# Optimization experiments

Hardware: AMD Instinct MI355X
Metric: run time of the kernel (lower is better)

## Reference

```python
import jax, jax.numpy as jnp
import numpy as np

VOXEL_SIZE = jnp.array([0.075, 0.075], dtype=jnp.float32)
PC_RANGE = jnp.array([-54.0, -54.0], dtype=jnp.float32)
FUSION_STRIDE = 8.0
SRC_STRIDES = (4.0, 8.0)
RADII = (2.4, 4.8)
NSAMPLE = 16
NKEY = 500


def _mlp(x, w1, g1, b1, w2, b2):
    # Linear(no bias) + BatchNorm(eval, running mean=0/var=1 -> affine) + ReLU, then Linear
    h = jax.nn.relu((x @ w1) * g1 + b1)
    return h @ w2 + b2


def _world(coords, stride):
    # voxel coord -> world xy center
    return (coords.astype(jnp.float32) + 0.5) * stride * VOXEL_SIZE + PC_RANGE


def _gather_rows(x, idx):
    # x: (B, N, ...), idx: (B, ...) -> per-batch row gather
    return jax.vmap(lambda f, i: f[i])(x, idx)


def _knn(key_world, src_world, src_feat, radius):
    # key_world (B,Nk,2), src_world (B,Ns,2), src_feat (B,Ns,C)
    d2 = jnp.sum((key_world[:, :, None, :] - src_world[:, None, :, :]) ** 2, axis=-1)  # (B,Nk,Ns)
    d2 = jnp.where(d2 <= radius * radius, d2, jnp.inf)
    negd, idx = jax.lax.top_k(-d2, NSAMPLE)  # nearest NSAMPLE within radius, (B,Nk,K)
    valid = jnp.isfinite(negd).astype(src_feat.dtype)  # empty==0 mask
    feats = _gather_rows(src_feat, idx)  # (B,Nk,K,C)
    return feats * valid[..., None]


def setup_inputs() -> dict:
    key = jax.random.key(0)
    ks = jax.random.split(key, 24)
    s = 0.05
    return {
        'fusion_feat': jax.random.normal(ks[0], (2, 20000, 128), jnp.float32),
        'src_feat_a': jax.random.normal(ks[1], (2, 30000, 128), jnp.float32),
        'src_feat_b': jax.random.normal(ks[2], (2, 30000, 128), jnp.float32),
        'heat_w1': jax.random.normal(ks[3], (128, 128), jnp.float32) * s,
        'heat_g1': jnp.ones((128,), jnp.float32),
        'heat_b1': jnp.zeros((128,), jnp.float32),
        'heat_w2': jax.random.normal(ks[4], (128, 10), jnp.float32) * s,
        'heat_b2': jnp.zeros((10,), jnp.float32),
        'knn_w': jax.random.normal(ks[5], (2, 16), jnp.float32) * s,
        'knn_b': jnp.zeros((2,), jnp.float32),
        'kw_w1': jax.random.normal(ks[6], (128, 64), jnp.float32) * s,
        'kw_g1': jnp.ones((64,), jnp.float32),
        'kw_b1': jnp.zeros((64,), jnp.float32),
        'kw_w2': jax.random.normal(ks[7], (64, 3), jnp.float32) * s,
        'kw_b2': jnp.zeros((3,), jnp.float32),
        'fuse_w1': jax.random.normal(ks[8], (256, 256), jnp.float32) * s,
        'fuse_g1': jnp.ones((256,), jnp.float32),
        'fuse_b1': jnp.zeros((256,), jnp.float32),
        'fuse_w2': jax.random.normal(ks[9], (256, 128), jnp.float32) * s,
        'fuse_b2': jnp.zeros((128,), jnp.float32),
        'fusion_coords': jax.random.randint(ks[10], (2, 20000, 2), 0, 180, jnp.int32),
        'src_coords_a': jax.random.randint(ks[11], (2, 30000, 2), 0, 360, jnp.int32),
        'src_coords_b': jax.random.randint(ks[12], (2, 30000, 2), 0, 180, jnp.int32),
    }


def reference(fusion_feat, src_feat_a, src_feat_b, heat_w1, heat_g1, heat_b1,
              heat_w2, heat_b2, knn_w, knn_b, kw_w1, kw_g1, kw_b1, kw_w2, kw_b2,
              fuse_w1, fuse_g1, fuse_b1, fuse_w2, fuse_b2,
              fusion_coords, src_coords_a, src_coords_b):
    B = fusion_feat.shape[0]
    # heatmap head over all fusion voxels
    scores10 = _mlp(fusion_feat, heat_w1, heat_g1, heat_b1, heat_w2, heat_b2)  # (B,Nf,10)
    heat_scores = jnp.max(scores10, axis=-1)
    cls = jnp.argmax(scores10, axis=-1)
    # per-sample top-k key voxel selection
    _, tki = jax.lax.top_k(jax.nn.sigmoid(heat_scores), NKEY)  # (B,Nk)
    key_feat = _gather_rows(fusion_feat, tki)      # (B,Nk,128)
    key_coords = _gather_rows(fusion_coords, tki)  # (B,Nk,2)
    key_class = _gather_rows(cls, tki)             # (B,Nk)
    key_world = _world(key_coords, FUSION_STRIDE)  # (B,Nk,2)

    srcs = ((src_feat_a, src_coords_a), (src_feat_b, src_coords_b))
    mlp_feats = []
    for s, (sf, sc) in enumerate(srcs):
        sw = _world(sc, SRC_STRIDES[s])
        kf = _knn(key_world, sw, sf, RADII[s])  # (B,Nk,K,C), zeroed where empty
        # Linear over the K neighbor axis (knn_feat_mlp: NSAMPLE -> 1)
        mf = jnp.einsum('bnkc,k->bnc', kf, knn_w[s]) + knn_b[s]
        mlp_feats.append(mf)

    w = jax.nn.softmax(_mlp(key_feat, kw_w1, kw_g1, kw_b1, kw_w2, kw_b2), axis=-1)  # (B,Nk,3)
    # faithful to original: key_voxel_feat is re-scaled cumulatively inside the loop
    kvf = key_feat
    fuse_sum = jnp.zeros_like(key_feat)
    for i in range(len(srcs)):
        kvf = w[..., i:i + 1] * kvf
        fuse_sum = fuse_sum + kvf * mlp_feats[i]
    fused = jnp.concatenate([fuse_sum, kvf], axis=-1)  # (B,Nk,256)
    out = _mlp(fused, fuse_w1, fuse_g1, fuse_b1, fuse_w2, fuse_b2)  # (B,Nk,128)

    bs_col = jnp.broadcast_to(jnp.arange(B, dtype=key_coords.dtype)[:, None, None], (B, NKEY, 1))
    key_voxel_indices = jnp.concatenate([bs_col, key_coords], axis=-1).reshape(B * NKEY, 3)
    return (out.reshape(B * NKEY, -1), key_voxel_indices,
            heat_scores.reshape(-1), scores10.reshape(-1, scores10.shape[-1]), key_class)
```

## Files before the change

### kernel.cpp

```cpp
#include <hip/hip_runtime.h>
#include <math.h>

#define BB 2
#define NF 20000
#define NS 30000
#define CH 128
#define NK 500
#define KNN 16
#define KPB 4

#define HA 2.4024f
#define HB 4.8048f
#define NCA 45
#define NCB 23
#define CELLS_A 2025
#define CELLS_B 529

#define OUT0_OFF 0
#define OUT1_OFF 128000
#define OUT2_OFF 131000
#define OUT3_OFF 171000
#define OUT4_OFF 571000

#define WS_CLS   0
#define WS_TKI   160000
#define WS_KW    164000
#define WS_MF    172000
#define WS_KEYS  WS_MF
#define WS_GSTART 1196000
#define WS_PTS    1236880
#define WS_PIDX   2196880

#define STB(s,b)  ((s) ? (4052 + (b) * 530) : ((b) * 2026))

__device__ __forceinline__ void fma4(float4& acc, float sc, const float4& wv) {
    acc.x += sc * wv.x; acc.y += sc * wv.y;
    acc.z += sc * wv.z; acc.w += sc * wv.w;
}

__device__ __forceinline__ unsigned ordf(float s) {
    unsigned u = __float_as_uint(s);
    return (u & 0x80000000u) ? ~u : (u | 0x80000000u);
}

__global__ __launch_bounds__(256) void heat_kernel(
    const float* __restrict__ x,
    const float* __restrict__ w1,
    const float* __restrict__ g1, const float* __restrict__ b1,
    const float* __restrict__ w2,
    const float* __restrict__ b2,
    float* __restrict__ out_heat,
    float* __restrict__ out_s10,
    int* __restrict__ cls,
    unsigned long long* __restrict__ keys)
{
    __shared__ float As[64 * 72];
    __shared__ float Ws[64 * 132];
    __shared__ float W2s[1280];
    const int tid = threadIdx.x;
    const int m0 = blockIdx.x * 64;
    const int tx = tid & 15;
    const int ty = tid >> 4;

    for (int v = tid; v < 1280; v += 256) W2s[v] = w2[v];

    float acc[4][8];
#pragma unroll
    for (int i = 0; i < 4; ++i)
#pragma unroll
        for (int j = 0; j < 8; ++j) acc[i][j] = 0.f;

    const float4* xv = (const float4*)x;
    const float4* w1v = (const float4*)w1;

    for (int kc = 0; kc < 128; kc += 64) {
#pragma unroll
        for (int i = 0; i < 4; ++i) {
            int v = tid + i * 256;
            int row = v >> 4, c4 = v & 15;
            float4 val = xv[(size_t)(m0 + row) * 32 + (kc >> 2) + c4];
            *(float4*)&As[row * 72 + c4 * 4] = val;
        }
#pragma unroll
        for (int i = 0; i < 8; ++i) {
            int v = tid + i * 256;
            int k = v >> 5, c4 = v & 31;
            float4 val = w1v[(size_t)(kc + k) * 32 + c4];
            *(float4*)&Ws[k * 132 + c4 * 4] = val;
        }
        __syncthreads();

        const float* a0p = &As[(ty * 4 + 0) * 72];
        const float* a1p = &As[(ty * 4 + 1) * 72];
        const float* a2p = &As[(ty * 4 + 2) * 72];
        const float* a3p = &As[(ty * 4 + 3) * 72];
#pragma unroll 4
        for (int k = 0; k < 64; ++k) {
            float4 bA = *(const float4*)&Ws[k * 132 + tx * 8];
            float4 bB = *(const float4*)&Ws[k * 132 + tx * 8 + 4];
            float a0 = a0p[k], a1 = a1p[k], a2 = a2p[k], a3 = a3p[k];
            acc[0][0] += a0 * bA.x; acc[0][1] += a0 * bA.y; acc[0][2] += a0 * bA.z; acc[0][3] += a0 * bA.w;
            acc[0][4] += a0 * bB.x; acc[0][5] += a0 * bB.y; acc[0][6] += a0 * bB.z; acc[0][7] += a0 * bB.w;
            acc[1][0] += a1 * bA.x; acc[1][1] += a1 * bA.y; acc[1][2] += a1 * bA.z; acc[1][3] += a1 * bA.w;
            acc[1][4] += a1 * bB.x; acc[1][5] += a1 * bB.y; acc[1][6] += a1 * bB.z; acc[1][7] += a1 * bB.w;
            acc[2][0] += a2 * bA.x; acc[2][1] += a2 * bA.y; acc[2][2] += a2 * bA.z; acc[2][3] += a2 * bA.w;
            acc[2][4] += a2 * bB.x; acc[2][5] += a2 * bB.y; acc[2][6] += a2 * bB.z; acc[2][7] += a2 * bB.w;
            acc[3][0] += a3 * bA.x; acc[3][1] += a3 * bA.y; acc[3][2] += a3 * bA.z; acc[3][3] += a3 * bA.w;
            acc[3][4] += a3 * bB.x; acc[3][5] += a3 * bB.y; acc[3][6] += a3 * bB.z; acc[3][7] += a3 * bB.w;
        }
        __syncthreads();
    }

    float4 g1a = ((const float4*)g1)[tx * 2], g1b = ((const float4*)g1)[tx * 2 + 1];
    float4 b1a = ((const float4*)b1)[tx * 2], b1b = ((const float4*)b1)[tx * 2 + 1];
    float* Hs = Ws;
#pragma unroll
    for (int i = 0; i < 4; ++i) {
        int row = ty * 4 + i;
        float4 hA, hB;
        hA.x = fmaxf(acc[i][0] * g1a.x + b1a.x, 0.f);
        hA.y = fmaxf(acc[i][1] * g1a.y + b1a.y, 0.f);
        hA.z = fmaxf(acc[i][2] * g1a.z + b1a.z, 0.f);
        hA.w = fmaxf(acc[i][3] * g1a.w + b1a.w, 0.f);
        hB.x = fmaxf(acc[i][4] * g1b.x + b1b.x, 0.f);
        hB.y = fmaxf(acc[i][5] * g1b.y + b1b.y, 0.f);
        hB.z = fmaxf(acc[i][6] * g1b.z + b1b.z, 0.f);
        hB.w = fmaxf(acc[i][7] * g1b.w + b1b.w, 0.f);
        *(float4*)&Hs[row * 132 + tx * 8] = hA;
        *(float4*)&Hs[row * 132 + tx * 8 + 4] = hB;
    }
    __syncthreads();

    const int r = tid >> 2;
    const int p = tid & 3;
    float a2[10];
#pragma unroll
    for (int c = 0; c < 10; ++c) a2[c] = 0.f;
    for (int kk = 0; kk < 32; ++kk) {
        int k = kk * 4 + p;
        float hv = Hs[r * 132 + k];
#pragma unroll
        for (int c = 0; c < 10; ++c) a2[c] += hv * W2s[k * 10 + c];
    }
#pragma unroll
    for (int c = 0; c < 10; ++c) {
        a2[c] += __shfl_xor(a2[c], 1);
        a2[c] += __shfl_xor(a2[c], 2);
    }
    if (p == 0) {
        int m = m0 + r;
        float best = -INFINITY;
        int bi = 0;
#pragma unroll
        for (int c = 0; c < 10; ++c) {
            float s = a2[c] + b2[c];
            out_s10[(size_t)m * 10 + c] = s;
            if (s > best) { best = s; bi = c; }
        }
        out_heat[m] = best;
        cls[m] = bi;
        int b = m / NF;
        unsigned i = (unsigned)(m - b * NF);
        float sig = 1.0f / (1.0f + expf(-best));
        keys[m] = ((unsigned long long)ordf(sig) << 32) | (unsigned)(~i);
    }
}

#define H1BINS 16384
#define H2BINS 1024

__device__ __forceinline__ void world_cell_sb(
    const int2* sc, int s, int i, float& sx, float& sy, int& cell)
{
    int2 c = sc[i];
    float stride = s ? 8.0f : 4.0f;
    sx = __fadd_rn(__fmul_rn(__fmul_rn(__fadd_rn((float)c.x, 0.5f), stride), 0.075f), -54.0f);
    sy = __fadd_rn(__fmul_rn(__fmul_rn(__fadd_rn((float)c.y, 0.5f), stride), 0.075f), -54.0f);
    float inv_h = s ? (1.0f / HB) : (1.0f / HA);
    int nc = s ? NCB : NCA;
    int cx = (int)floorf((sx + 54.0f) * inv_h);
    int cy = (int)floorf((sy + 54.0f) * inv_h);
    cx = min(max(cx, 0), nc - 1);
    cy = min(max(cy, 0), nc - 1);
    cell = cy * nc + cx;
}

__global__ __launch_bounds__(1024) void mid_kernel(
    const unsigned long long* __restrict__ keys,
    const int* __restrict__ cls,
    const int* __restrict__ fcoords,
    float* __restrict__ out1,
    float* __restrict__ out4,
    int* __restrict__ tki,
    float* __restrict__ keyworld,
    const int* __restrict__ sca, const int* __restrict__ scb,
    int* __restrict__ gstart,
    float2* __restrict__ pts, int* __restrict__ pidx)
{
    __shared__ unsigned h[H1BINS];
    __shared__ unsigned long long list[1024];
    __shared__ unsigned csum[1024];
    __shared__ unsigned ssum[32];
    __shared__ unsigned sel_s, krem_s, cnt_s;
    __shared__ int ghist[2048];
    __shared__ int gt0[1024], gt1[1024];
    const int tid = threadIdx.x;
    const int blk = blockIdx.x;

    if (blk >= 2) {
        const int s = (blk - 2) >> 1, b = (blk - 2) & 1;
        const int n = s ? CELLS_B : CELLS_A;
        const int stb = STB(s, b);
        const int2* sc = ((const int2*)(s ? scb : sca)) + (size_t)b * NS;
        const size_t pbase = ((size_t)s * BB + b) * NS;

        for (int i = tid; i < 2048; i += 1024) ghist[i] = 0;
        __syncthreads();
        for (int i = tid; i < NS; i += 1024) {
            float sx, sy; int cell;
            world_cell_sb(sc, s, i, sx, sy, cell);
            atomicAdd(&ghist[cell], 1);
        }
        __syncthreads();
        int i0 = tid * 2, i1 = tid * 2 + 1;
        int c0 = (i0 < n) ? ghist[i0] : 0;
        int c1 = (i1 < n) ? ghist[i1] : 0;
        gt0[tid] = c0 + c1;
        __syncthreads();
        int* srcp = gt0; int* dstp = gt1;
        for (int off = 1; off < 1024; off <<= 1) {
            int v = srcp[tid];
            if (tid >= off) v += srcp[tid - off];
            dstp[tid] = v;
            __syncthreads();
            int* tmp = srcp; srcp = dstp; dstp = tmp;
        }
        int excl = (tid == 0) ? 0 : srcp[tid - 1];
        if (i0 < n) { gstart[stb + i0] = excl; ghist[i0] = excl; }
        if (i1 < n) { gstart[stb + i1] = excl + c0; ghist[i1] = excl + c0; }
        if (tid == 0) gstart[stb + n] = NS;
        __syncthreads();
        for (int i = tid; i < NS; i += 1024) {
            float sx, sy; int cell;
            world_cell_sb(sc, s, i, sx, sy, cell);
            int pos = atomicAdd(&ghist[cell], 1);
            pts[pbase + pos] = make_float2(sx, sy);
            pidx[pbase + pos] = i;
        }
        return;
    }

    const int b = blk;
    const unsigned long long* kb = keys + (size_t)b * NF;

    for (int i = tid; i < H1BINS; i += 1024) h[i] = 0u;
    __syncthreads();
#pragma unroll 4
    for (int i = tid; i < NF; i += 1024)
        atomicAdd(&h[(unsigned)(kb[i] >> 50)], 1u);
    __syncthreads();
    {
        unsigned s = 0;
        int base = tid * 16;
#pragma unroll
        for (int j = 0; j < 16; ++j) s += h[base + j];
        csum[tid] = s;
    }
    __syncthreads();
    if (tid < 32) {
        unsigned s = 0;
        for (int j = 0; j < 32; ++j) s += csum[tid * 32 + j];
        ssum[tid] = s;
    }
    __syncthreads();
    if (tid == 0) {
        unsigned K = NK, acc = 0;
        int sidx = 31;
        for (; sidx > 0; --sidx) { if (acc + ssum[sidx] >= K) break; acc += ssum[sidx]; }
        int cidx = sidx * 32 + 31;
        for (;; --cidx) { if (acc + csum[cidx] >= K) break; acc += csum[cidx]; }
        int bin = cidx * 16 + 15;
        for (;; --bin) { if (acc + h[bin] >= K) break; acc += h[bin]; }
        sel_s = (unsigned)bin;
        krem_s = K - acc;
    }
    __syncthreads();
    const unsigned T1 = sel_s;
    const unsigned K2 = krem_s;

    for (int i = tid; i < H2BINS; i += 1024) h[i] = 0u;
    __syncthreads();
#pragma unroll 4
    for (int i = tid; i < NF; i += 1024) {
        unsigned long long key = kb[i];
        if ((unsigned)(key >> 50) == T1)
            atomicAdd(&h[(unsigned)(key >> 40) & 1023u], 1u);
    }
    __syncthreads();
    if (tid < 32) {
        unsigned s = 0;
        for (int j = 0; j < 32; ++j) s += h[tid * 32 + j];
        csum[tid] = s;
    }
    __syncthreads();
    if (tid == 0) {
        unsigned acc = 0;
        int cidx = 31;
        for (; cidx > 0; --cidx) { if (acc + csum[cidx] >= K2) break; acc += csum[cidx]; }
        int bin = cidx * 32 + 31;
        for (;; --bin) { if (acc + h[bin] >= K2) break; acc += h[bin]; }
        sel_s = (T1 << 10) | (unsigned)bin;
        cnt_s = 0u;
    }
    __syncthreads();
    const unsigned thr24 = sel_s;

#pragma unroll 4
    for (int i = tid; i < NF; i += 1024) {
        unsigned long long key = kb[i];
        if ((unsigned)(key >> 40) >= thr24) {
            unsigned pos = atomicAdd(&cnt_s, 1u);
            if (pos < 1024u) list[pos] = key;
        }
    }
    __syncthreads();
    unsigned cc = cnt_s > 1024u ? 1024u : cnt_s;
    if ((unsigned)tid >= cc) list[tid] = 0ull;
    __syncthreads();

    for (int kk = 2; kk <= 1024; kk <<= 1) {
        for (int j = kk >> 1; j > 0; j >>= 1) {
            int i = tid, ixj = i ^ j;
            if (ixj > i) {
                unsigned long long a = list[i], bv = list[ixj];
                bool up = ((i & kk) == 0);
                if (up ? (a < bv) : (a > bv)) { list[i] = bv; list[ixj] = a; }
            }
            __syncthreads();
        }
    }

    if (tid < NK) {
        unsigned long long key = list[tid];
        int idx = (int)(~(unsigned)(key & 0xFFFFFFFFull));
        tki[b * NK + tid] = idx;
        int c0 = fcoords[((size_t)b * NF + idx) * 2 + 0];
        int c1 = fcoords[((size_t)b * NF + idx) * 2 + 1];
        size_t o = (size_t)(b * NK + tid);
        out1[o * 3 + 0] = (float)b;
        out1[o * 3 + 1] = (float)c0;
        out1[o * 3 + 2] = (float)c1;
        float wx = __fadd_rn(__fmul_rn(__fmul_rn(__fadd_rn((float)c0, 0.5f), 8.0f), 0.075f), -54.0f);
        float wy = __fadd_rn(__fmul_rn(__fmul_rn(__fadd_rn((float)c1, 0.5f), 8.0f), 0.075f), -54.0f);
        keyworld[o * 2 + 0] = wx;
        keyworld[o * 2 + 1] = wy;
        out4[o] = (float)cls[(size_t)b * NF + idx];
    }
}

__global__ __launch_bounds__(256) void knn_kernel(
    const float* __restrict__ sfa, const float* __restrict__ sfb,
    const int* __restrict__ gstart,
    const float2* __restrict__ pts, const int* __restrict__ pidx,
    const float* __restrict__ knn_w,
    const float* __restrict__ knn_b,
    const float* __restrict__ keyworld,
    float* __restrict__ mf)
{
    __shared__ unsigned long long list[1024];
    __shared__ float psum[128];
    __shared__ unsigned cnt_s;
    const int tid = threadIdx.x;
    const int blk = blockIdx.x;
    const int s = blk / (BB * NK);
    const int rest = blk % (BB * NK);
    const int b = rest / NK;
    const int r = rest % NK;
    const float* sfeat = s ? sfb : sfa;
    const float r2 = s ? (float)(4.8 * 4.8) : (float)(2.4 * 2.4);
    const float inv_h = s ? (1.0f / HB) : (1.0f / HA);
    const int nc = s ? NCB : NCA;
    const int stb = STB(s, b);
    const size_t pbase = ((size_t)s * BB + b) * NS;

    if (tid == 0) cnt_s = 0u;
    __syncthreads();
    const float kx = keyworld[((size_t)b * NK + r) * 2 + 0];
    const float ky = keyworld[((size_t)b * NK + r) * 2 + 1];
    int cx = (int)floorf((kx + 54.0f) * inv_h);
    int cy = (int)floorf((ky + 54.0f) * inv_h);
    cx = min(max(cx, 0), nc - 1);
    cy = min(max(cy, 0), nc - 1);
    const int c0 = max(cx - 1, 0), c1 = min(cx + 1, nc - 1);
    const int cy0 = max(cy - 1, 0), cy1 = min(cy + 1, nc - 1);

    for (int cyy = cy0; cyy <= cy1; ++cyy) {
        int lo = gstart[stb + cyy * nc + c0];
        int hi = gstart[stb + cyy * nc + c1 + 1];
        for (int p = lo + tid; p < hi; p += 256) {
            float2 w = pts[pbase + p];
            float dx = __fsub_rn(kx, w.x);
            float dy = __fsub_rn(ky, w.y);
            float d2 = __fadd_rn(__fmul_rn(dx, dx), __fmul_rn(dy, dy));
            if (d2 <= r2) {
                unsigned pos = atomicAdd(&cnt_s, 1u);
                if (pos < 1024u)
                    list[pos] = ((unsigned long long)__float_as_uint(d2) << 32)
                              | (unsigned)pidx[pbase + p];
            }
        }
    }
    __syncthreads();
    int cc = (int)cnt_s;
    if (cc > 1024) cc = 1024;
    int n2 = 16;
    while (n2 < cc) n2 <<= 1;
    for (int i = tid; i < n2; i += 256)
        if (i >= cc) list[i] = ~0ull;
    __syncthreads();
    for (int kk = 2; kk <= n2; kk <<= 1) {
        for (int j = kk >> 1; j > 0; j >>= 1) {
            for (int i = tid; i < n2; i += 256) {
                int ixj = i ^ j;
                if (ixj > i) {
                    unsigned long long a = list[i], bv = list[ixj];
                    bool up = ((i & kk) == 0);
                    bool sw = up ? (a > bv) : (a < bv);
                    if (sw) { list[i] = bv; list[ixj] = a; }
                }
            }
            __syncthreads();
        }
    }
    {
        int K = cc < KNN ? cc : KNN;
        int col = tid & 127, half = tid >> 7;
        float acc = 0.f;
        int k0 = half * 8, k1 = min(K, half * 8 + 8);
        for (int k = k0; k < k1; ++k) {
            unsigned i = (unsigned)(list[k] & 0xFFFFFFFFull);
            acc += knn_w[s * 16 + k] * sfeat[((size_t)b * NS + i) * CH + col];
        }
        if (half) psum[col] = acc;
        __syncthreads();
        if (!half)
            mf[(((size_t)s * BB + b) * NK + r) * CH + col] = knn_b[s] + acc + psum[col];
    }
}

__global__ __launch_bounds__(1024) void fuse_kernel(
    const float* __restrict__ ffeat,
    const int* __restrict__ tki,
    const float* __restrict__ kw_w1, const float* __restrict__ kw_g1,
    const float* __restrict__ kw_b1, const float* __restrict__ kw_w2,
    const float* __restrict__ kw_b2,
    const float* __restrict__ fuse_w1, const float* __restrict__ fuse_g1,
    const float* __restrict__ fuse_b1, const float* __restrict__ fuse_w2,
    const float* __restrict__ fuse_b2,
    const float* __restrict__ mf,
    float* __restrict__ out0)
{
    __shared__ float pL[16384];
    __shared__ float xsT[512];
    __shared__ float mfs[1024];
    __shared__ float fusedvT[1024];
    __shared__ float h2sT[1024];
    __shared__ float prm[964];
    __shared__ float hsX[256];
    __shared__ float p2[96];
    __shared__ float l3[12];
    __shared__ float wsm[8];
    __shared__ int idxs[KPB], bs[KPB], rs[KPB];
    const int tid = threadIdx.x;
    const int f0 = blockIdx.x * KPB;

    if (tid < 964) {
        float v;
        if (tid < 64)       v = kw_g1[tid];
        else if (tid < 128) v = kw_b1[tid - 64];
        else if (tid < 320) v = kw_w2[tid - 128];
        else if (tid < 323) v = kw_b2[tid - 320];
        else if (tid < 324) v = 0.f;
        else if (tid < 580) v = fuse_g1[tid - 324];
        else if (tid < 836) v = fuse_b1[tid - 580];
        else                v = fuse_b2[tid - 836];
        prm[tid] = v;
    }
    if (tid < KPB) {
        int flat = f0 + tid;
        int b = flat / NK;
        bs[tid] = b;
        rs[tid] = flat - b * NK;
        idxs[tid] = tki[flat];
    }
    __syncthreads();

    if (tid < 128) {
        int key = tid >> 5, c4 = tid & 31;
        float4 v = ((const float4*)(ffeat + ((size_t)bs[key] * NF + idxs[key]) * CH))[c4];
        xsT[(c4 * 4 + 0) * 4 + key] = v.x;
        xsT[(c4 * 4 + 1) * 4 + key] = v.y;
        xsT[(c4 * 4 + 2) * 4 + key] = v.z;
        xsT[(c4 * 4 + 3) * 4 + key] = v.w;
    }
    if (tid < 256) {
        int ss = tid >> 7, key = (tid >> 5) & 3, c4 = tid & 31;
        float4 v = ((const float4*)(mf + (((size_t)ss * BB + bs[key]) * NK + rs[key]) * CH))[c4];
        *(float4*)&mfs[ss * 512 + key * 128 + c4 * 4] = v;
    }
    __syncthreads();

    if (tid < 256) {
        const int og = tid & 15, kseg = tid >> 4;
        float4 wr[8];
#pragma unroll
        for (int m = 0; m < 8; ++m)
            wr[m] = ((const float4*)kw_w1)[(kseg * 8 + m) * 16 + og];
        float4 a0 = {0, 0, 0, 0}, a1 = {0, 0, 0, 0}, a2 = {0, 0, 0, 0}, a3 = {0, 0, 0, 0};
#pragma unroll
        for (int m = 0; m < 8; ++m) {
            float4 f4 = *(const float4*)&xsT[(kseg * 8 + m) * 4];
            fma4(a0, f4.x, wr[m]);
            fma4(a1, f4.y, wr[m]);
            fma4(a2, f4.z, wr[m]);
            fma4(a3, f4.w, wr[m]);
        }
        *(float4*)&pL[(kseg * 4 + 0) * 64 + og * 4] = a0;
        *(float4*)&pL[(kseg * 4 + 1) * 64 + og * 4] = a1;
        *(float4*)&pL[(kseg * 4 + 2) * 64 + og * 4] = a2;
        *(float4*)&pL[(kseg * 4 + 3) * 64 + og * 4] = a3;
    }
    __syncthreads();
    if (tid < 256) {
        int out = tid >> 2, key = tid & 3;
        float s = 0.f;
#pragma unroll
        for (int ks = 0; ks < 16; ++ks) s += pL[(ks * 4 + key) * 64 + out];
        float t = s * prm[out] + prm[64 + out];
        hsX[key * 64 + out] = t > 0.f ? t : 0.f;
    }
    __syncthreads();
    if (tid < 96) {
        int key = tid / 24, rr = tid % 24, out = rr >> 3, seg = rr & 7;
        float acc = 0.f;
#pragma unroll
        for (int m = 0; m < 8; ++m) {
            int k = seg * 8 + m;
            acc += hsX[key * 64 + k] * prm[128 + k * 3 + out];
        }
        p2[(key * 3 + out) * 8 + seg] = acc;
    }
    __syncthreads();
    if (tid < 12) {
        int key = tid / 3, out = tid % 3;
        float s = 0.f;
#pragma unroll
        for (int j = 0; j < 8; ++j) s += p2[(key * 3 + out) * 8 + j];
        l3[key * 3 + out] = s + prm[320 + out];
    }
    __syncthreads();
    if (tid < KPB) {
        float l0 = l3[tid * 3], l1 = l3[tid * 3 + 1], l2 = l3[tid * 3 + 2];
        float m = fmaxf(l0, fmaxf(l1, l2));
        float e0 = expf(l0 - m), e1 = expf(l1 - m), e2 = expf(l2 - m);
        float sum = e0 + e1 + e2;
        wsm[tid * 2 + 0] = e0 / sum;
        wsm[tid * 2 + 1] = e1 / sum;
    }
    __syncthreads();

    {
        int c = tid >> 2, key = tid & 3;
        float w0 = wsm[key * 2], w1_ = wsm[key * 2 + 1];
        float val;
        if (c < 128) {
            float xv_ = xsT[c * 4 + key];
            float m0 = mfs[key * 128 + c];
            float m1 = mfs[512 + key * 128 + c];
            float kv = w0 * xv_;
            float kv2 = w1_ * kv;
            val = kv * m0 + kv2 * m1;
        } else {
            float xv_ = xsT[(c - 128) * 4 + key];
            val = w1_ * (w0 * xv_);
        }
        fusedvT[tid] = val;
    }
    __syncthreads();

    {
        const int og = tid & 63, kseg = tid >> 6;
        const float4* w1v = (const float4*)fuse_w1;
        float4 wr[16];
#pragma unroll
        for (int m = 0; m < 16; ++m)
            wr[m] = w1v[(kseg * 16 + m) * 64 + og];
        float4 a0 = {0, 0, 0, 0}, a1 = {0, 0, 0, 0}, a2 = {0, 0, 0, 0}, a3 = {0, 0, 0, 0};
#pragma unroll
        for (int m = 0; m < 16; ++m) {
            float4 f4 = *(const float4*)&fusedvT[(kseg * 16 + m) * 4];
            fma4(a0, f4.x, wr[m]);
            fma4(a1, f4.y, wr[m]);
            fma4(a2, f4.z, wr[m]);
            fma4(a3, f4.w, wr[m]);
        }
        *(float4*)&pL[(kseg * 4 + 0) * 256 + og * 4] = a0;
        *(float4*)&pL[(kseg * 4 + 1) * 256 + og * 4] = a1;
        *(float4*)&pL[(kseg * 4 + 2) * 256 + og * 4] = a2;
        *(float4*)&pL[(kseg * 4 + 3) * 256 + og * 4] = a3;
    }
    __syncthreads();
    {
        int out = tid >> 2, key = tid & 3;
        float s = 0.f;
#pragma unroll
        for (int ks = 0; ks < 16; ++ks) s += pL[(ks * 4 + key) * 256 + out];
        float t = s * prm[324 + out] + prm[580 + out];
        h2sT[out * 4 + key] = t > 0.f ? t : 0.f;
    }
    __syncthreads();

    {
        const int og2 = tid & 31, kseg2 = tid >> 5;
        const float4* w2v = (const float4*)fuse_w2;
        float4 wr[8];
#pragma unroll
        for (int m = 0; m < 8; ++m)
            wr[m] = w2v[(kseg2 * 8 + m) * 32 + og2];
        float4 a0 = {0, 0, 0, 0}, a1 = {0, 0, 0, 0}, a2 = {0, 0, 0, 0}, a3 = {0, 0, 0, 0};
#pragma unroll
        for (int m = 0; m < 8; ++m) {
            float4 f4 = *(const float4*)&h2sT[(kseg2 * 8 + m) * 4];
            fma4(a0, f4.x, wr[m]);
            fma4(a1, f4.y, wr[m]);
            fma4(a2, f4.z, wr[m]);
            fma4(a3, f4.w, wr[m]);
        }
        *(float4*)&pL[(kseg2 * 4 + 0) * 128 + og2 * 4] = a0;
        *(float4*)&pL[(kseg2 * 4 + 1) * 128 + og2 * 4] = a1;
        *(float4*)&pL[(kseg2 * 4 + 2) * 128 + og2 * 4] = a2;
        *(float4*)&pL[(kseg2 * 4 + 3) * 128 + og2 * 4] = a3;
    }
    __syncthreads();
    if (tid < 512) {
        int out = tid >> 2, key = tid & 3;
        float s = prm[836 + out];
#pragma unroll
        for (int ks = 0; ks < 32; ++ks) s += pL[(ks * 4 + key) * 128 + out];
        out0[((size_t)bs[key] * NK + rs[key]) * CH + out] = s;
    }
}

extern "C" void kernel_launch(void* const* d_in, const int* in_sizes, int n_in,
                              void* d_out, int out_size, void* d_ws, size_t ws_size,
                              hipStream_t stream)
{
    const float* fusion_feat = (const float*)d_in[0];
    const float* src_feat_a  = (const float*)d_in[1];
    const float* src_feat_b  = (const float*)d_in[2];
    const float* heat_w1 = (const float*)d_in[3];
    const float* heat_g1 = (const float*)d_in[4];
    const float* heat_b1 = (const float*)d_in[5];
    const float* heat_w2 = (const float*)d_in[6];
    const float* heat_b2 = (const float*)d_in[7];
    const float* knn_w   = (const float*)d_in[8];
    const float* knn_b   = (const float*)d_in[9];
    const float* kw_w1   = (const float*)d_in[10];
    const float* kw_g1   = (const float*)d_in[11];
    const float* kw_b1   = (const float*)d_in[12];
    const float* kw_w2   = (const float*)d_in[13];
    const float* kw_b2   = (const float*)d_in[14];
    const float* fuse_w1 = (const float*)d_in[15];
    const float* fuse_g1 = (const float*)d_in[16];
    const float* fuse_b1 = (const float*)d_in[17];
    const float* fuse_w2 = (const float*)d_in[18];
    const float* fuse_b2 = (const float*)d_in[19];
    const int* fusion_coords = (const int*)d_in[20];
    const int* src_coords_a  = (const int*)d_in[21];
    const int* src_coords_b  = (const int*)d_in[22];

    float* out = (float*)d_out;
    char* ws = (char*)d_ws;
    int* cls = (int*)(ws + WS_CLS);
    int* tki = (int*)(ws + WS_TKI);
    float* keyworld = (float*)(ws + WS_KW);
    float* mf = (float*)(ws + WS_MF);
    unsigned long long* keys = (unsigned long long*)(ws + WS_KEYS);
    int* gstart = (int*)(ws + WS_GSTART);
    float2* pts = (float2*)(ws + WS_PTS);
    int* pidx = (int*)(ws + WS_PIDX);

    heat_kernel<<<(BB * NF) / 64, 256, 0, stream>>>(
        fusion_feat, heat_w1, heat_g1, heat_b1, heat_w2, heat_b2,
        out + OUT2_OFF, out + OUT3_OFF, cls, keys);

    mid_kernel<<<6, 1024, 0, stream>>>(
        keys, cls, fusion_coords,
        out + OUT1_OFF, out + OUT4_OFF, tki, keyworld,
        src_coords_a, src_coords_b, gstart, pts, pidx);

    knn_kernel<<<2 * BB * NK, 256, 0, stream>>>(
        src_feat_a, src_feat_b, gstart, pts, pidx,
        knn_w, knn_b, keyworld, mf);

    fuse_kernel<<<(BB * NK) / KPB, 1024, 0, stream>>>(
        fusion_feat, tki, kw_w1, kw_g1, kw_b1, kw_w2, kw_b2,
        fuse_w1, fuse_g1, fuse_b1, fuse_w2, fuse_b2, mf, out + OUT0_OFF);
}
```

Baseline: 245.3 us.

## Move grid-binning into heat kernel and streamline top-k selection

The source-point grid binning (histogram, scan, scatter) moves out of the serial mid kernel into four extra blocks of the heat kernel, so it overlaps with the heat MLP instead of running after it. The top-k kernel now finds the threshold bin with a parallel suffix scan instead of serial loops. It skips the second histogram pass when the first-level candidates fit in the list. It also replaces the 1024-element bitonic sort with a rank-by-count placement over the candidates. This shortens the latency-bound single-block section between kernels, but the binning now runs with 256 threads per block instead of 1024. The O(n^2) ranking assumes distinct keys.

```diff
diff --git a/kernel.cpp b/kernel.cpp
--- a/kernel.cpp
+++ b/kernel.cpp
@@ -33,6 +33,8 @@
 
 #define STB(s,b)  ((s) ? (4052 + (b) * 530) : ((b) * 2026))
 
+#define HEATBLKS 625
+
 __device__ __forceinline__ void fma4(float4& acc, float sc, const float4& wv) {
     acc.x += sc * wv.x; acc.y += sc * wv.y;
     acc.z += sc * wv.z; acc.w += sc * wv.w;
@@ -41,6 +43,22 @@
 __device__ __forceinline__ unsigned ordf(float s) {
     unsigned u = __float_as_uint(s);
     return (u & 0x80000000u) ? ~u : (u | 0x80000000u);
+}
+
+__device__ __forceinline__ void world_cell_sb(
+    const int2* sc, int s, int i, float& sx, float& sy, int& cell)
+{
+    int2 c = sc[i];
+    float stride = s ? 8.0f : 4.0f;
+    sx = __fadd_rn(__fmul_rn(__fmul_rn(__fadd_rn((float)c.x, 0.5f), stride), 0.075f), -54.0f);
+    sy = __fadd_rn(__fmul_rn(__fmul_rn(__fadd_rn((float)c.y, 0.5f), stride), 0.075f), -54.0f);
+    float inv_h = s ? (1.0f / HB) : (1.0f / HA);
+    int nc = s ? NCB : NCA;
+    int cx = (int)floorf((sx + 54.0f) * inv_h);
+    int cy = (int)floorf((sy + 54.0f) * inv_h);
+    cx = min(max(cx, 0), nc - 1);
+    cy = min(max(cy, 0), nc - 1);
+    cell = cy * nc + cx;
 }
 
 __global__ __launch_bounds__(256) void heat_kernel(
@@ -52,12 +70,69 @@
     float* __restrict__ out_heat,
     float* __restrict__ out_s10,
     int* __restrict__ cls,
-    unsigned long long* __restrict__ keys)
+    unsigned long long* __restrict__ keys,
+    const int* __restrict__ sca, const int* __restrict__ scb,
+    int* __restrict__ gstart,
+    float2* __restrict__ pts, int* __restrict__ pidx)
 {
     __shared__ float As[64 * 72];
     __shared__ float Ws[64 * 132];
     __shared__ float W2s[1280];
     const int tid = threadIdx.x;
+
+    if (blockIdx.x >= HEATBLKS) {
+        const int g = blockIdx.x - HEATBLKS;
+        const int s = g >> 1, b = g & 1;
+        const int n = s ? CELLS_B : CELLS_A;
+        const int stb = STB(s, b);
+        const int2* sc = ((const int2*)(s ? scb : sca)) + (size_t)b * NS;
+        const size_t pbase = ((size_t)s * BB + b) * NS;
+        int* ghist = (int*)As;
+        int* ct  = (int*)Ws;
+        int* ct2 = ((int*)Ws) + 256;
+
+        for (int i = tid; i < 2048; i += 256) ghist[i] = 0;
+        __syncthreads();
+        for (int i = tid; i < NS; i += 256) {
+            float sx, sy; int cell;
+            world_cell_sb(sc, s, i, sx, sy, cell);
+            atomicAdd(&ghist[cell], 1);
+        }
+        __syncthreads();
+        const int base = tid * 8;
+        int loc[8]; int csum8 = 0;
+#pragma unroll
+        for (int j = 0; j < 8; ++j) { loc[j] = ghist[base + j]; csum8 += loc[j]; }
+        ct[tid] = csum8;
+        __syncthreads();
+        int* srcp = ct; int* dstp = ct2;
+        for (int off = 1; off < 256; off <<= 1) {
+            int v = srcp[tid];
+            if (tid >= off) v += srcp[tid - off];
+            dstp[tid] = v;
+            __syncthreads();
+            int* t = srcp; srcp = dstp; dstp = t;
+        }
+        int excl = (tid == 0) ? 0 : srcp[tid - 1];
+        __syncthreads();
+#pragma unroll
+        for (int j = 0; j < 8; ++j) {
+            if (base + j < n) gstart[stb + base + j] = excl;
+            ghist[base + j] = excl;
+            excl += loc[j];
+        }
+        if (tid == 0) gstart[stb + n] = NS;
+        __syncthreads();
+        for (int i = tid; i < NS; i += 256) {
+            float sx, sy; int cell;
+            world_cell_sb(sc, s, i, sx, sy, cell);
+            int pos = atomicAdd(&ghist[cell], 1);
+            pts[pbase + pos] = make_float2(sx, sy);
+            pidx[pbase + pos] = i;
+        }
+        return;
+    }
+
     const int m0 = blockIdx.x * 64;
     const int tx = tid & 15;
     const int ty = tid >> 4;
@@ -167,91 +242,24 @@
 }
 
 #define H1BINS 16384
-#define H2BINS 1024
-
-__device__ __forceinline__ void world_cell_sb(
-    const int2* sc, int s, int i, float& sx, float& sy, int& cell)
-{
-    int2 c = sc[i];
-    float stride = s ? 8.0f : 4.0f;
-    sx = __fadd_rn(__fmul_rn(__fmul_rn(__fadd_rn((float)c.x, 0.5f), stride), 0.075f), -54.0f);
-    sy = __fadd_rn(__fmul_rn(__fmul_rn(__fadd_rn((float)c.y, 0.5f), stride), 0.075f), -54.0f);
-    float inv_h = s ? (1.0f / HB) : (1.0f / HA);
-    int nc = s ? NCB : NCA;
-    int cx = (int)floorf((sx + 54.0f) * inv_h);
-    int cy = (int)floorf((sy + 54.0f) * inv_h);
-    cx = min(max(cx, 0), nc - 1);
-    cy = min(max(cy, 0), nc - 1);
-    cell = cy * nc + cx;
-}
-
-__global__ __launch_bounds__(1024) void mid_kernel(
+
+__global__ __launch_bounds__(1024) void topk_kernel(
     const unsigned long long* __restrict__ keys,
     const int* __restrict__ cls,
     const int* __restrict__ fcoords,
     float* __restrict__ out1,
     float* __restrict__ out4,
     int* __restrict__ tki,
-    float* __restrict__ keyworld,
-    const int* __restrict__ sca, const int* __restrict__ scb,
-    int* __restrict__ gstart,
-    float2* __restrict__ pts, int* __restrict__ pidx)
+    float* __restrict__ keyworld)
 {
     __shared__ unsigned h[H1BINS];
+    __shared__ unsigned sA[1024], sB[1024];
     __shared__ unsigned long long list[1024];
-    __shared__ unsigned csum[1024];
-    __shared__ unsigned ssum[32];
-    __shared__ unsigned sel_s, krem_s, cnt_s;
-    __shared__ int ghist[2048];
-    __shared__ int gt0[1024], gt1[1024];
+    __shared__ unsigned chunk_s, aboveC_s, T1_s, aboveT1_s, cand_s, thr_s, cnt_s;
+    const int b = blockIdx.x;
     const int tid = threadIdx.x;
-    const int blk = blockIdx.x;
-
-    if (blk >= 2) {
-        const int s = (blk - 2) >> 1, b = (blk - 2) & 1;
-        const int n = s ? CELLS_B : CELLS_A;
-        const int stb = STB(s, b);
-        const int2* sc = ((const int2*)(s ? scb : sca)) + (size_t)b * NS;
-        const size_t pbase = ((size_t)s * BB + b) * NS;
-
-        for (int i = tid; i < 2048; i += 1024) ghist[i] = 0;
-        __syncthreads();
-        for (int i = tid; i < NS; i += 1024) {
-            float sx, sy; int cell;
-            world_cell_sb(sc, s, i, sx, sy, cell);
-            atomicAdd(&ghist[cell], 1);
-        }
-        __syncthreads();
-        int i0 = tid * 2, i1 = tid * 2 + 1;
-        int c0 = (i0 < n) ? ghist[i0] : 0;
-        int c1 = (i1 < n) ? ghist[i1] : 0;
-        gt0[tid] = c0 + c1;
-        __syncthreads();
-        int* srcp = gt0; int* dstp = gt1;
-        for (int off = 1; off < 1024; off <<= 1) {
-            int v = srcp[tid];
-            if (tid >= off) v += srcp[tid - off];
-            dstp[tid] = v;
-            __syncthreads();
-            int* tmp = srcp; srcp = dstp; dstp = tmp;
-        }
-        int excl = (tid == 0) ? 0 : srcp[tid - 1];
-        if (i0 < n) { gstart[stb + i0] = excl; ghist[i0] = excl; }
-        if (i1 < n) { gstart[stb + i1] = excl + c0; ghist[i1] = excl + c0; }
-        if (tid == 0) gstart[stb + n] = NS;
-        __syncthreads();
-        for (int i = tid; i < NS; i += 1024) {
-            float sx, sy; int cell;
-            world_cell_sb(sc, s, i, sx, sy, cell);
-            int pos = atomicAdd(&ghist[cell], 1);
-            pts[pbase + pos] = make_float2(sx, sy);
-            pidx[pbase + pos] = i;
-        }
-        return;
-    }
-
-    const int b = blk;
     const unsigned long long* kb = keys + (size_t)b * NF;
+    const unsigned K = NK;
 
     for (int i = tid; i < H1BINS; i += 1024) h[i] = 0u;
     __syncthreads();
@@ -259,102 +267,110 @@
     for (int i = tid; i < NF; i += 1024)
         atomicAdd(&h[(unsigned)(kb[i] >> 50)], 1u);
     __syncthreads();
+    unsigned ck = 0;
     {
-        unsigned s = 0;
         int base = tid * 16;
 #pragma unroll
-        for (int j = 0; j < 16; ++j) s += h[base + j];
-        csum[tid] = s;
-    }
-    __syncthreads();
-    if (tid < 32) {
-        unsigned s = 0;
-        for (int j = 0; j < 32; ++j) s += csum[tid * 32 + j];
-        ssum[tid] = s;
+        for (int j = 0; j < 16; ++j) ck += h[base + j];
+        sA[tid] = ck;
+    }
+    __syncthreads();
+    unsigned* srcp = sA; unsigned* dstp = sB;
+    for (int off = 1; off < 1024; off <<= 1) {
+        unsigned v = srcp[tid];
+        if (tid + off < 1024) v += srcp[tid + off];
+        dstp[tid] = v;
+        __syncthreads();
+        unsigned* t = srcp; srcp = dstp; dstp = t;
+    }
+    {
+        unsigned suf = srcp[tid];
+        unsigned above = suf - ck;
+        if (above < K && K <= suf) { chunk_s = (unsigned)tid; aboveC_s = above; }
     }
     __syncthreads();
     if (tid == 0) {
-        unsigned K = NK, acc = 0;
-        int sidx = 31;
-        for (; sidx > 0; --sidx) { if (acc + ssum[sidx] >= K) break; acc += ssum[sidx]; }
-        int cidx = sidx * 32 + 31;
-        for (;; --cidx) { if (acc + csum[cidx] >= K) break; acc += csum[cidx]; }
-        int bin = cidx * 16 + 15;
+        int bin = (int)chunk_s * 16 + 15;
+        unsigned acc = aboveC_s;
         for (;; --bin) { if (acc + h[bin] >= K) break; acc += h[bin]; }
-        sel_s = (unsigned)bin;
-        krem_s = K - acc;
-    }
-    __syncthreads();
-    const unsigned T1 = sel_s;
-    const unsigned K2 = krem_s;
-
-    for (int i = tid; i < H2BINS; i += 1024) h[i] = 0u;
-    __syncthreads();
+        T1_s = (unsigned)bin;
+        aboveT1_s = acc;
+        cand_s = acc + h[bin];
+        cnt_s = 0u;
+    }
+    __syncthreads();
+    const unsigned T1 = T1_s;
+
+    if (cand_s <= 1024u) {
 #pragma unroll 4
-    for (int i = tid; i < NF; i += 1024) {
-        unsigned long long key = kb[i];
-        if ((unsigned)(key >> 50) == T1)
-            atomicAdd(&h[(unsigned)(key >> 40) & 1023u], 1u);
-    }
-    __syncthreads();
-    if (tid < 32) {
-        unsigned s = 0;
-        for (int j = 0; j < 32; ++j) s += h[tid * 32 + j];
-        csum[tid] = s;
-    }
-    __syncthreads();
-    if (tid == 0) {
-        unsigned acc = 0;
-        int cidx = 31;
-        for (; cidx > 0; --cidx) { if (acc + csum[cidx] >= K2) break; acc += csum[cidx]; }
-        int bin = cidx * 32 + 31;
-        for (;; --bin) { if (acc + h[bin] >= K2) break; acc += h[bin]; }
-        sel_s = (T1 << 10) | (unsigned)bin;
-        cnt_s = 0u;
-    }
-    __syncthreads();
-    const unsigned thr24 = sel_s;
-
+        for (int i = tid; i < NF; i += 1024) {
+            unsigned long long key = kb[i];
+            if ((unsigned)(key >> 50) >= T1) {
+                unsigned pos = atomicAdd(&cnt_s, 1u);
+                if (pos < 1024u) list[pos] = key;
+            }
+        }
+    } else {
+        const unsigned K2 = K - aboveT1_s;
+        h[tid] = 0u;
+        __syncthreads();
 #pragma unroll 4
-    for (int i = tid; i < NF; i += 1024) {
-        unsigned long long key = kb[i];
-        if ((unsigned)(key >> 40) >= thr24) {
-            unsigned pos = atomicAdd(&cnt_s, 1u);
-            if (pos < 1024u) list[pos] = key;
-        }
-    }
-    __syncthreads();
-    unsigned cc = cnt_s > 1024u ? 1024u : cnt_s;
-    if ((unsigned)tid >= cc) list[tid] = 0ull;
-    __syncthreads();
-
-    for (int kk = 2; kk <= 1024; kk <<= 1) {
-        for (int j = kk >> 1; j > 0; j >>= 1) {
-            int i = tid, ixj = i ^ j;
-            if (ixj > i) {
-                unsigned long long a = list[i], bv = list[ixj];
-                bool up = ((i & kk) == 0);
-                if (up ? (a < bv) : (a > bv)) { list[i] = bv; list[ixj] = a; }
+        for (int i = tid; i < NF; i += 1024) {
+            unsigned long long key = kb[i];
+            if ((unsigned)(key >> 50) == T1)
+                atomicAdd(&h[(unsigned)(key >> 40) & 1023u], 1u);
+        }
+        __syncthreads();
+        unsigned hb = h[tid];
+        sA[tid] = hb;
+        __syncthreads();
+        unsigned* s2 = sA; unsigned* d2 = sB;
+        for (int off = 1; off < 1024; off <<= 1) {
+            unsigned v = s2[tid];
+            if (tid + off < 1024) v += s2[tid + off];
+            d2[tid] = v;
+            __syncthreads();
+            unsigned* t = s2; s2 = d2; d2 = t;
+        }
+        {
+            unsigned suf = s2[tid];
+            unsigned above = suf - hb;
+            if (above < K2 && K2 <= suf) thr_s = (T1 << 10) | (unsigned)tid;
+        }
+        __syncthreads();
+        const unsigned thr24 = thr_s;
+#pragma unroll 4
+        for (int i = tid; i < NF; i += 1024) {
+            unsigned long long key = kb[i];
+            if ((unsigned)(key >> 40) >= thr24) {
+                unsigned pos = atomicAdd(&cnt_s, 1u);
+                if (pos < 1024u) list[pos] = key;
             }
-            __syncthreads();
-        }
-    }
-
-    if (tid < NK) {
-        unsigned long long key = list[tid];
-        int idx = (int)(~(unsigned)(key & 0xFFFFFFFFull));
-        tki[b * NK + tid] = idx;
-        int c0 = fcoords[((size_t)b * NF + idx) * 2 + 0];
-        int c1 = fcoords[((size_t)b * NF + idx) * 2 + 1];
-        size_t o = (size_t)(b * NK + tid);
-        out1[o * 3 + 0] = (float)b;
-        out1[o * 3 + 1] = (float)c0;
-        out1[o * 3 + 2] = (float)c1;
-        float wx = __fadd_rn(__fmul_rn(__fmul_rn(__fadd_rn((float)c0, 0.5f), 8.0f), 0.075f), -54.0f);
-        float wy = __fadd_rn(__fmul_rn(__fmul_rn(__fadd_rn((float)c1, 0.5f), 8.0f), 0.075f), -54.0f);
-        keyworld[o * 2 + 0] = wx;
-        keyworld[o * 2 + 1] = wy;
-        out4[o] = (float)cls[(size_t)b * NF + idx];
+        }
+    }
+    __syncthreads();
+    const int cc = (int)(cnt_s > 1024u ? 1024u : cnt_s);
+
+    if (tid < cc) {
+        unsigned long long mykey = list[tid];
+        unsigned r = 0;
+#pragma unroll 8
+        for (int j = 0; j < cc; ++j) r += (list[j] > mykey) ? 1u : 0u;
+        if (r < (unsigned)NK) {
+            int idx = (int)(~(unsigned)(mykey & 0xFFFFFFFFull));
+            tki[b * NK + (int)r] = idx;
+            int c0 = fcoords[((size_t)b * NF + idx) * 2 + 0];
+            int c1 = fcoords[((size_t)b * NF + idx) * 2 + 1];
+            size_t o = (size_t)(b * NK + (int)r);
+            out1[o * 3 + 0] = (float)b;
+            out1[o * 3 + 1] = (float)c0;
+            out1[o * 3 + 2] = (float)c1;
+            float wx = __fadd_rn(__fmul_rn(__fmul_rn(__fadd_rn((float)c0, 0.5f), 8.0f), 0.075f), -54.0f);
+            float wy = __fadd_rn(__fmul_rn(__fmul_rn(__fadd_rn((float)c1, 0.5f), 8.0f), 0.075f), -54.0f);
+            keyworld[o * 2 + 0] = wx;
+            keyworld[o * 2 + 1] = wy;
+            out4[o] = (float)cls[(size_t)b * NF + idx];
+        }
     }
 }
 
@@ -690,14 +706,14 @@
     float2* pts = (float2*)(ws + WS_PTS);
     int* pidx = (int*)(ws + WS_PIDX);
 
-    heat_kernel<<<(BB * NF) / 64, 256, 0, stream>>>(
+    heat_kernel<<<HEATBLKS + 4, 256, 0, stream>>>(
         fusion_feat, heat_w1, heat_g1, heat_b1, heat_w2, heat_b2,
-        out + OUT2_OFF, out + OUT3_OFF, cls, keys);
-
-    mid_kernel<<<6, 1024, 0, stream>>>(
+        out + OUT2_OFF, out + OUT3_OFF, cls, keys,
+        src_coords_a, src_coords_b, gstart, pts, pidx);
+
+    topk_kernel<<<BB, 1024, 0, stream>>>(
         keys, cls, fusion_coords,
-        out + OUT1_OFF, out + OUT4_OFF, tki, keyworld,
-        src_coords_a, src_coords_b, gstart, pts, pidx);
+        out + OUT1_OFF, out + OUT4_OFF, tki, keyworld);
 
     knn_kernel<<<2 * BB * NK, 256, 0, stream>>>(
         src_feat_a, src_feat_b, gstart, pts, pidx,
```

Measured after the change: 298.5 us. +21.7%, slower.
